# Performance work log

Hardware: AMD Instinct MI355X
Metric: run time of the kernel (lower is better)

Reference implementation:

```python
import jax, jax.numpy as jnp
import numpy as np

N = 200000
E = 600000
H = 128
OUT = 256
NUM_TYPES = 300
B = 128


def setup_inputs() -> dict:
    key = jax.random.key(0)
    ks = jax.random.split(key, 12)
    x = jax.random.randint(ks[0], (N,), 0, NUM_TYPES)
    edge_index = jax.random.randint(ks[1], (2, E), 0, N)
    batch = jnp.sort(jax.random.randint(ks[2], (N,), 0, B))
    s = 1.0 / np.sqrt(H)
    emb = jax.random.normal(ks[3], (NUM_TYPES, H), jnp.float32)
    W0 = jax.random.uniform(ks[4], (H, H), jnp.float32, -s, s)
    b0 = jax.random.uniform(ks[5], (H,), jnp.float32, -s, s)
    W1 = jax.random.uniform(ks[6], (H, H), jnp.float32, -s, s)
    b1 = jax.random.uniform(ks[7], (H,), jnp.float32, -s, s)
    Wo = jax.random.uniform(ks[8], (H, OUT), jnp.float32, -s, s)
    bo = jax.random.uniform(ks[9], (OUT,), jnp.float32, -s, s)
    gamma = jnp.ones((OUT,), jnp.float32)
    beta = jnp.zeros((OUT,), jnp.float32)
    return {"x": x, "edge_index": edge_index, "batch": batch, "batch_size": B,
            "emb": emb, "W0": W0, "b0": b0, "W1": W1, "b1": b1,
            "Wo": Wo, "bo": bo, "gamma": gamma, "beta": beta}


def gcn_layer(h, full_src, full_dst, W, b, n):
    # gather messages, scatter-add to destinations (bidirectional edges pre-built)
    msg = h[full_src]                                   # [2E, H]
    agg = jax.ops.segment_sum(msg, full_dst, num_segments=n)
    deg = jax.ops.segment_sum(jnp.ones((full_src.shape[0],), h.dtype),
                              full_dst, num_segments=n)
    deg = jnp.sqrt(jnp.clip(deg, 1.0))[:, None]
    out = agg / deg
    out = out @ W + b
    out = out + h
    return jax.nn.gelu(out, approximate=False)  # torch nn.GELU default is exact


def reference(x, edge_index, batch, batch_size, emb, W0, b0, W1, b1, Wo, bo, gamma, beta):
    n = x.shape[0]
    h = emb[x]                                          # [N, H] embedding gather
    src, dst = edge_index[0], edge_index[1]
    full_src = jnp.concatenate([src, dst])
    full_dst = jnp.concatenate([dst, src])
    h = gcn_layer(h, full_src, full_dst, W0, b0, n)
    h = gcn_layer(h, full_src, full_dst, W1, b1, n)
    # segment-mean pooling per graph
    gsum = jax.ops.segment_sum(h, batch, num_segments=batch_size)
    cnt = jax.ops.segment_sum(jnp.ones((n,), h.dtype), batch, num_segments=batch_size)
    gfeat = gsum / jnp.clip(cnt, 1.0)[:, None]
    out = gfeat @ Wo + bo
    mu = jnp.mean(out, axis=-1, keepdims=True)
    var = jnp.var(out, axis=-1, keepdims=True)
    out = (out - mu) * jax.lax.rsqrt(var + 1e-5) * gamma + beta
    return out
```

## Files before the change

### kernel.cpp

```cpp
#include <hip/hip_runtime.h>
#include <hip/hip_bf16.h>
#include <hip/hip_fp8.h>
#include <math.h>

#define H 128
#define OUTD 256
#define ASTRIDE 40
#define NODE_MASK 0x3FFFF

typedef unsigned short ushort_t;
typedef unsigned int uint_t;
typedef unsigned char uchar_t;
typedef __attribute__((ext_vector_type(8))) short short8;
typedef __attribute__((ext_vector_type(4))) float f32x4;
typedef __attribute__((ext_vector_type(2))) float f32x2;

__device__ __forceinline__ float bf2f(uint_t u){
    union { uint_t i; float f; } v; v.i = u << 16; return v.f;
}
__device__ __forceinline__ uint_t f2bf(float f){
    __hip_bfloat16 b = __float2bfloat16(f);
    union { __hip_bfloat16 b; ushort_t u; } v; v.b = b; return (uint_t)v.u;
}
__device__ __forceinline__ float fp8tof(uint_t u){
    __hip_fp8_e4m3 t; t.__x = (__hip_fp8_storage_t)u; return (float)t;
}
__device__ __forceinline__ uint_t ftofp8(float f){
    __hip_fp8_e4m3 t(f); return (uint_t)t.__x;
}
__device__ __forceinline__ uint_t pk2fp8(float a, float b){
#if __has_builtin(__builtin_amdgcn_cvt_pk_fp8_f32)
    return (uint_t)__builtin_amdgcn_cvt_pk_fp8_f32(a, b, 0, false) & 0xFFFFu;
#else
    return ftofp8(a) | (ftofp8(b) << 8);
#endif
}
__device__ __forceinline__ void acc_fp8(f32x4& v, uint_t u){
#if __has_builtin(__builtin_amdgcn_cvt_pk_f32_fp8)
    f32x2 lo = __builtin_amdgcn_cvt_pk_f32_fp8(u, false);
    f32x2 hi = __builtin_amdgcn_cvt_pk_f32_fp8(u, true);
    v[0] += lo[0]; v[1] += lo[1]; v[2] += hi[0]; v[3] += hi[1];
#else
    v[0] += fp8tof(u & 0xFFu);         v[1] += fp8tof((u >> 8) & 0xFFu);
    v[2] += fp8tof((u >> 16) & 0xFFu); v[3] += fp8tof(u >> 24);
#endif
}
__device__ __forceinline__ float gelu_fast(float x){
    float a = fabsf(x) * 0.70710678118654752440f;
    float t = __builtin_amdgcn_rcpf(fmaf(0.3275911f, a, 1.0f));
    float p = t*fmaf(t, fmaf(t, fmaf(t, fmaf(t, 1.061405429f, -1.453152027f),
                                     1.421413741f), -0.284496736f), 0.254829592f);
    float erf = 1.0f - p*__expf(-a*a);
    erf = copysignf(erf, x);
    return 0.5f * x * (1.0f + erf);
}

__global__ __launch_bounds__(256) void sniff_kernel(const ushort_t* __restrict__ data,
                                                    int count, int* __restrict__ flag_fp32){
    __shared__ float red[256];
    float m = 0.f;
    for (int i = threadIdx.x; i < count; i += 256){
        float v = fabsf(bf2f((uint_t)data[i]));
        if (isfinite(v)) m = fmaxf(m, v);
        else m = 1e30f;
    }
    red[threadIdx.x] = m;
    __syncthreads();
    #pragma unroll
    for (int s = 128; s > 0; s >>= 1){
        if (threadIdx.x < s) red[threadIdx.x] = fmaxf(red[threadIdx.x], red[threadIdx.x+s]);
        __syncthreads();
    }
    if (threadIdx.x == 0) *flag_fp32 = (red[0] > 100.f) ? 1 : 0;
}

struct StageArgs {
    const void* src[7];
    float*      dst[7];
    int         count[7];
    int         blk_off[8];
};
__global__ __launch_bounds__(256) void stage_all_kernel(StageArgs args,
                                                        const int* __restrict__ flag_fp32){
    int bx = blockIdx.x;
    int seg = 0;
    while (seg < 6 && bx >= args.blk_off[seg+1]) seg++;
    int idx = (bx - args.blk_off[seg])*256 + threadIdx.x;
    if (idx >= args.count[seg]) return;
    const int isf32 = *flag_fp32;
    args.dst[seg][idx] = isf32 ? ((const float*)args.src[seg])[idx]
                               : bf2f((uint_t)((const ushort_t*)args.src[seg])[idx]);
}

__global__ __launch_bounds__(256) void transpose_w_kernel(
        const void* __restrict__ Ws0, const void* __restrict__ Ws1,
        const void* __restrict__ embsrc, int szEmb,
        ushort_t* __restrict__ d0, ushort_t* __restrict__ d1,
        ushort_t* __restrict__ dEmb, uchar_t* __restrict__ dEmb8,
        int* __restrict__ zero_base, int zero_count,
        const int* __restrict__ flag_fp32){
    if (blockIdx.y == 3){
        for (int i = blockIdx.x*256 + threadIdx.x; i < zero_count; i += gridDim.x*256)
            zero_base[i] = 0;
        return;
    }
    const int isf32 = *flag_fp32;
    if (blockIdx.y == 2){
        int i = blockIdx.x*256 + threadIdx.x;
        if (i >= szEmb) return;
        ushort_t bv = isf32 ? (ushort_t)f2bf(((const float*)embsrc)[i])
                            : ((const ushort_t*)embsrc)[i];
        dEmb[i] = bv;
        int row = i >> 7, col = i & 127;
        int kb = col >> 5, qq = (col >> 3) & 3, jj = col & 7;
        dEmb8[(size_t)row*H + qq*32 + kb*8 + jj] = (uchar_t)ftofp8(bf2f((uint_t)bv));
        return;
    }
    const void* s = blockIdx.y ? Ws1 : Ws0;
    ushort_t*   d = blockIdx.y ? d1  : d0;
    int i = blockIdx.x*256 + threadIdx.x;
    if (i >= H*H) return;
    int k = i >> 7, nn = i & 127;
    ushort_t v = isf32 ? (ushort_t)f2bf(((const float*)s)[i])
                       : ((const ushort_t*)s)[i];
    d[nn*H + k] = v;
}

__global__ __launch_bounds__(256) void fill_part_kernel(const int* __restrict__ src,
        const int* __restrict__ dst, const int* __restrict__ x,
        int* __restrict__ deg, int* __restrict__ adj, int E, int n){
    int group = blockIdx.x & 7;
    int gblk  = blockIdx.x >> 3;
    int G     = gridDim.x >> 3;
    int lo = (int)(((long long)n * group) / 8);
    int hi = (int)(((long long)n * (group+1)) / 8);
    for (int e = gblk*256 + threadIdx.x; e < E; e += G*256){
        int s = src[e], d = dst[e];
        if (d >= lo && d < hi){
            int ts = x[s];
            int p = atomicAdd(&deg[d], 1);
            if (p < ASTRIDE) adj[(size_t)d*ASTRIDE + p] = s | (ts << 18);
        }
        if (s >= lo && s < hi){
            int td = x[d];
            int p = atomicAdd(&deg[s], 1);
            if (p < ASTRIDE) adj[(size_t)s*ASTRIDE + p] = d | (td << 18);
        }
    }
}

__global__ __launch_bounds__(512, 6) void gcn_fused(
    const int* __restrict__ deg, const int* __restrict__ adj,
    const ushort_t* __restrict__ gsrc, const uchar_t* __restrict__ g8,
    const int* __restrict__ xmap,
    const ushort_t* __restrict__ WT, const float* __restrict__ b,
    ushort_t* __restrict__ h_out, uchar_t* __restrict__ h8_out,
    int n, int use_x){
    __shared__ ushort_t Wt[128*136];
    for (int i = threadIdx.x; i < 2048; i += 512){
        int nn = i >> 4;
        int k0 = (i & 15) << 3;
        *(uint4*)(&Wt[nn*136 + k0]) = *(const uint4*)(WT + nn*H + k0);
    }
    __syncthreads();
    const int lane = threadIdx.x & 63;
    const int wave = threadIdx.x >> 6;
    const int quad = lane >> 4;
    const int lid  = lane & 15;

    int row = blockIdx.x*128 + wave*16 + lid;
    int cnt = (row < n) ? deg[row] : 0;
    float s = rsqrtf((float)(cnt < 1 ? 1 : cnt));
    if (cnt > ASTRIDE) cnt = ASTRIDE;
    const uint_t* ap = (const uint_t*)(adj + (size_t)row*ASTRIDE);

    f32x4 g[8];
    #pragma unroll
    for (int i=0;i<8;i++) g[i] = (f32x4){0.f,0.f,0.f,0.f};

    uint4 c0 = {0,0,0,0}, c1 = {0,0,0,0}, n0 = {0,0,0,0}, n1 = {0,0,0,0};
    if (cnt > 0){
        uint_t e = ap[0];
        size_t ro = (size_t)(use_x ? (e >> 18) : (e & NODE_MASK)) * H;
        const uchar_t* hp = g8 + ro + quad*32;
        c0 = *(const uint4*)(hp); c1 = *(const uint4*)(hp + 16);
    }
    if (cnt > 1){
        uint_t e = ap[1];
        size_t ro = (size_t)(use_x ? (e >> 18) : (e & NODE_MASK)) * H;
        const uchar_t* hp = g8 + ro + quad*32;
        n0 = *(const uint4*)(hp); n1 = *(const uint4*)(hp + 16);
    }
    for (int j=0; j<cnt; j++){
        uint4 f0 = {0,0,0,0}, f1 = {0,0,0,0};
        if (j+2 < cnt){
            uint_t e = ap[j+2];
            size_t ro = (size_t)(use_x ? (e >> 18) : (e & NODE_MASK)) * H;
            const uchar_t* hp = g8 + ro + quad*32;
            f0 = *(const uint4*)(hp); f1 = *(const uint4*)(hp + 16);
        }
        acc_fp8(g[0], c0.x); acc_fp8(g[1], c0.y);
        acc_fp8(g[2], c0.z); acc_fp8(g[3], c0.w);
        acc_fp8(g[4], c1.x); acc_fp8(g[5], c1.y);
        acc_fp8(g[6], c1.z); acc_fp8(g[7], c1.w);
        c0 = n0; c1 = n1; n0 = f0; n1 = f1;
    }

    short8 afrag[4];
    #pragma unroll
    for (int kb=0;kb<4;kb++){
        uint_t w0 = f2bf(g[2*kb][0]*s)   | (f2bf(g[2*kb][1]*s)   << 16);
        uint_t w1 = f2bf(g[2*kb][2]*s)   | (f2bf(g[2*kb][3]*s)   << 16);
        uint_t w2 = f2bf(g[2*kb+1][0]*s) | (f2bf(g[2*kb+1][1]*s) << 16);
        uint_t w3 = f2bf(g[2*kb+1][2]*s) | (f2bf(g[2*kb+1][3]*s) << 16);
        uint4 packed; packed.x=w0; packed.y=w1; packed.z=w2; packed.w=w3;
        afrag[kb] = *(short8*)&packed;
    }

    f32x4 acc[8];
    #pragma unroll
    for (int ct=0;ct<8;ct++) acc[ct] = (f32x4){0.f,0.f,0.f,0.f};
    #pragma unroll
    for (int kb=0;kb<4;kb++){
        #pragma unroll
        for (int ct=0;ct<8;ct++){
            short8 bf = *(const short8*)(&Wt[(ct*16+lid)*136 + kb*32 + quad*8]);
            acc[ct] = __builtin_amdgcn_mfma_f32_16x16x32_bf16(afrag[kb], bf, acc[ct], 0,0,0);
        }
    }

    float bcol[8];
    #pragma unroll
    for (int ct=0;ct<8;ct++) bcol[ct] = b[ct*16 + lid];
    int rowq = blockIdx.x*128 + wave*16 + quad*4;
    bool full = (blockIdx.x*128 + wave*16 + 16) <= n;
    const int boff = ((lid >> 3) << 5) + (lid & 7);
    #pragma unroll
    for (int r=0;r<4;r++){
        int grow = rowq + r;
        if (full || grow < n){
            if (use_x){
                const ushort_t* hr = gsrc + (size_t)xmap[grow]*H + lid;
                uchar_t* o8 = h8_out + (size_t)grow*H;
                float vv[8];
                #pragma unroll
                for (int ct=0;ct<8;ct++){
                    float hv = bf2f((uint_t)hr[ct*16]);
                    vv[ct] = gelu_fast(acc[ct][r] + bcol[ct] + hv);
                }
                #pragma unroll
                for (int cp=0;cp<4;cp++){
                    uint_t pk = pk2fp8(vv[2*cp], vv[2*cp+1]);
                    o8[boff + cp*8]      = (uchar_t)(pk & 0xFF);
                    o8[boff + 64 + cp*8] = (uchar_t)(pk >> 8);
                }
            } else {
                const uchar_t* h8r = g8 + (size_t)grow*H;
                ushort_t* orp = h_out + (size_t)grow*H + lid;
                #pragma unroll
                for (int ct=0;ct<8;ct++){
                    int off2 = boff + ((ct & 1) << 6) + ((ct >> 1) << 3);
                    float hv = fp8tof((uint_t)h8r[off2]);
                    float v  = gelu_fast(acc[ct][r] + bcol[ct] + hv);
                    orp[ct*16] = (ushort_t)f2bf(v);
                }
            }
        }
    }
}

__global__ __launch_bounds__(256) void pool_kernel(const ushort_t* __restrict__ h,
        const int* __restrict__ batch, float* __restrict__ gfeat, int n){
    int g = blockIdx.x;
    int q = blockIdx.y;
    __shared__ int se[2];
    if (threadIdx.x == 0){
        int lo=0, hi=n;
        while (lo<hi){ int m=(lo+hi)>>1; if (batch[m] < g) lo=m+1; else hi=m; }
        se[0] = lo;
        hi = n;
        while (lo<hi){ int m=(lo+hi)>>1; if (batch[m] <= g) lo=m+1; else hi=m; }
        se[1] = lo;
    }
    __syncthreads();
    int start = se[0], end = se[1];
    int chunk = (end - start + 3) >> 2;
    int s = start + q*chunk;
    int e = s + chunk; if (e > end) e = end;
    int col0 = (threadIdx.x & 15) << 3;
    int rg   = threadIdx.x >> 4;
    float acc[8];
    #pragma unroll
    for (int i=0;i<8;i++) acc[i] = 0.f;
    for (int r = s + rg; r < e; r += 16){
        uint4 raw = *(const uint4*)(h + (size_t)r*H + col0);
        acc[0] += bf2f(raw.x & 0xFFFFu); acc[1] += bf2f(raw.x >> 16);
        acc[2] += bf2f(raw.y & 0xFFFFu); acc[3] += bf2f(raw.y >> 16);
        acc[4] += bf2f(raw.z & 0xFFFFu); acc[5] += bf2f(raw.z >> 16);
        acc[6] += bf2f(raw.w & 0xFFFFu); acc[7] += bf2f(raw.w >> 16);
    }
    __shared__ float red[16][128];
    #pragma unroll
    for (int i=0;i<8;i++) red[rg][col0+i] = acc[i];
    __syncthreads();
    #pragma unroll
    for (int st=8; st>=1; st>>=1){
        if (rg < st){
            #pragma unroll
            for (int i=0;i<8;i++) red[rg][col0+i] += red[rg+st][col0+i];
        }
        __syncthreads();
    }
    if (rg == 0){
        #pragma unroll
        for (int i=0;i<8;i++) atomicAdd(&gfeat[(size_t)g*H + col0 + i], red[0][col0+i]);
    }
}

__global__ __launch_bounds__(256) void head_kernel(const float* __restrict__ gfeat,
        const int* __restrict__ batch, int n,
        const float* __restrict__ Wo, const float* __restrict__ bo,
        const float* __restrict__ gamma, const float* __restrict__ beta,
        void* __restrict__ out, const int* __restrict__ flag_fp32){
    int g = blockIdx.x;
    int j = threadIdx.x;
    __shared__ float gf[H];
    __shared__ float icnt_sh;
    if (j == 0){
        int lo=0, hi=n;
        while (lo<hi){ int m=(lo+hi)>>1; if (batch[m] < g) lo=m+1; else hi=m; }
        int st = lo;
        hi = n;
        while (lo<hi){ int m=(lo+hi)>>1; if (batch[m] <= g) lo=m+1; else hi=m; }
        int cnt = lo - st; if (cnt < 1) cnt = 1;
        icnt_sh = 1.0f / (float)cnt;
    }
    __syncthreads();
    if (j < H) gf[j] = gfeat[(size_t)g*H + j] * icnt_sh;
    __syncthreads();
    float acc = bo[j];
    #pragma unroll 8
    for (int k=0;k<H;k++) acc += gf[k] * Wo[(size_t)k*OUTD + j];
    __shared__ float red[256];
    red[j] = acc;
    __syncthreads();
    #pragma unroll
    for (int s2=128;s2>0;s2>>=1){
        if (j < s2) red[j] += red[j+s2];
        __syncthreads();
    }
    float mu = red[0] * (1.f/OUTD);
    __syncthreads();
    float d = acc - mu;
    red[j] = d*d;
    __syncthreads();
    #pragma unroll
    for (int s2=128;s2>0;s2>>=1){
        if (j < s2) red[j] += red[j+s2];
        __syncthreads();
    }
    float var = red[0] * (1.f/OUTD);
    float val = d * rsqrtf(var + 1e-5f) * gamma[j] + beta[j];
    size_t idx = (size_t)g*OUTD + j;
    if (*flag_fp32) ((float*)out)[idx] = val;
    else            ((ushort_t*)out)[idx] = (ushort_t)f2bf(val);
}

extern "C" void kernel_launch(void* const* d_in, const int* in_sizes, int n_in,
                              void* d_out, int out_size, void* d_ws, size_t ws_size,
                              hipStream_t stream){
    const int* x     = (const int*)d_in[0];
    const int* edge  = (const int*)d_in[1];
    const int* batch = (const int*)d_in[2];

    const int n = in_sizes[0];
    const int E = in_sizes[1] / 2;
    const int B = out_size / OUTD;
    const int* srcp = edge;
    const int* dstp = edge + E;

    const int szEmb = in_sizes[4], szb0 = in_sizes[6], szb1 = in_sizes[8];
    const int szWo = in_sizes[9], szbo = in_sizes[10], szg = in_sizes[11], szbt = in_sizes[12];

    char* base = (char*)d_ws;
    size_t off = 0;
    auto take = [&](size_t bytes)->char*{
        char* p = base + off;
        off = (off + bytes + 15) & ~(size_t)15;
        return p;
    };
    int*   flag   = (int*)  take(4);
    ushort_t* embb= (ushort_t*)take((size_t)szEmb*2);
    uchar_t* emb8 = (uchar_t*)take((size_t)szEmb);
    ushort_t* WT0 = (ushort_t*)take((size_t)H*H*2);
    ushort_t* WT1 = (ushort_t*)take((size_t)H*H*2);
    float* sb0    = (float*)take((size_t)szb0*4);
    float* sb1    = (float*)take((size_t)szb1*4);
    float* sWo    = (float*)take((size_t)szWo*4);
    float* sbo    = (float*)take((size_t)szbo*4);
    float* sg     = (float*)take((size_t)szg*4);
    float* sbt    = (float*)take((size_t)szbt*4);
    int*   adj    = (int*)  take((size_t)n*ASTRIDE*4);
    ushort_t* hA  = (ushort_t*)take((size_t)n*H*2);
    uchar_t*  h8  = (uchar_t*)take((size_t)n*H);
    char* zbase   = take((size_t)n*4 + (size_t)B*H*4);
    int*   deg    = (int*)zbase;
    float* gfeat  = (float*)(zbase + (size_t)n*4);
    const int zero_ints = n + B*H;

    sniff_kernel<<<1, 256, 0, stream>>>((const ushort_t*)d_in[4], szEmb, flag);

    StageArgs sa;
    const void* ssrc[7] = {d_in[9], d_in[6], d_in[8], d_in[10], d_in[11], d_in[12], d_in[10]};
    float*      sdst[7] = {sWo, sb0, sb1, sbo, sg, sbt, sbo};
    int         scnt[7] = {szWo, szb0, szb1, szbo, szg, szbt, 0};
    int run = 0;
    for (int i=0;i<7;i++){
        sa.src[i] = ssrc[i]; sa.dst[i] = sdst[i]; sa.count[i] = scnt[i];
        sa.blk_off[i] = run; run += (scnt[i] + 255)/256;
    }
    sa.blk_off[7] = run;
    stage_all_kernel<<<run, 256, 0, stream>>>(sa, flag);
    int tgrid = ((H*H > szEmb ? H*H : szEmb) + 255)/256;
    transpose_w_kernel<<<dim3(tgrid, 4), 256, 0, stream>>>(d_in[5], d_in[7],
                                                           d_in[4], szEmb,
                                                           WT0, WT1, embb, emb8,
                                                           (int*)zbase, zero_ints, flag);

    fill_part_kernel<<<2048, 256, 0, stream>>>(srcp, dstp, x, deg, adj, E, n);

    const int nblk = (n + 127) / 128;
    gcn_fused<<<nblk, 512, 0, stream>>>(deg, adj, embb, emb8, x,
                                        WT0, sb0, (ushort_t*)nullptr, h8, n, 1);
    gcn_fused<<<nblk, 512, 0, stream>>>(deg, adj, embb, h8, x,
                                        WT1, sb1, hA, (uchar_t*)nullptr, n, 0);

    pool_kernel<<<dim3(B,4), 256, 0, stream>>>(hA, batch, gfeat, n);
    head_kernel<<<B, 256, 0, stream>>>(gfeat, batch, n, sWo, sbo, sg, sbt, d_out, flag);
}
```

Baseline: 351.8 us.

## Fuse mean-pool into second GCN layer and batch-prefetch neighbor gathers

The second GCN layer now adds its GELU outputs straight into per-block shared-memory pooling bins, falling back to global atomics for graphs outside the bins. This removes the bf16 hidden-state write and the separate pool kernel. The neighbor gather loads adjacency entries in vector chunks and issues four row gathers ahead, unrolled for the first 12 edges. The kernel is also templated on USE_X and launch bounds change from 6 to 4 blocks per SM, which trades occupancy for registers and adds shared-memory atomic contention.

```diff
diff --git a/kernel.cpp b/kernel.cpp
--- a/kernel.cpp
+++ b/kernel.cpp
@@ -7,6 +7,7 @@
 #define OUTD 256
 #define ASTRIDE 40
 #define NODE_MASK 0x3FFFF
+#define PBINS 4
 
 typedef unsigned short ushort_t;
 typedef unsigned int uint_t;
@@ -39,7 +40,9 @@
 #if __has_builtin(__builtin_amdgcn_cvt_pk_f32_fp8)
     f32x2 lo = __builtin_amdgcn_cvt_pk_f32_fp8(u, false);
     f32x2 hi = __builtin_amdgcn_cvt_pk_f32_fp8(u, true);
-    v[0] += lo[0]; v[1] += lo[1]; v[2] += hi[0]; v[3] += hi[1];
+    f32x2 a = {v[0], v[1]}, b2 = {v[2], v[3]};
+    a += lo; b2 += hi;
+    v = (f32x4){a[0], a[1], b2[0], b2[1]};
 #else
     v[0] += fp8tof(u & 0xFFu);         v[1] += fp8tof((u >> 8) & 0xFFu);
     v[2] += fp8tof((u >> 16) & 0xFFu); v[3] += fp8tof(u >> 24);
@@ -149,18 +152,37 @@
     }
 }
 
-__global__ __launch_bounds__(512, 6) void gcn_fused(
+#define GLOAD(E, RA, RB) do { \
+    size_t ro_ = (size_t)(USE_X ? ((E) >> 18) : ((E) & NODE_MASK)) * H; \
+    const uchar_t* hp_ = g8 + ro_ + quad*32; \
+    RA = *(const uint4*)(hp_); RB = *(const uint4*)(hp_ + 16); } while(0)
+
+#define GACC(RA, RB) do { \
+    acc_fp8(g[0], RA.x); acc_fp8(g[1], RA.y); \
+    acc_fp8(g[2], RA.z); acc_fp8(g[3], RA.w); \
+    acc_fp8(g[4], RB.x); acc_fp8(g[5], RB.y); \
+    acc_fp8(g[6], RB.z); acc_fp8(g[7], RB.w); } while(0)
+
+template<int USE_X>
+__global__ __launch_bounds__(512, 4) void gcn_fused(
     const int* __restrict__ deg, const int* __restrict__ adj,
     const ushort_t* __restrict__ gsrc, const uchar_t* __restrict__ g8,
     const int* __restrict__ xmap,
     const ushort_t* __restrict__ WT, const float* __restrict__ b,
-    ushort_t* __restrict__ h_out, uchar_t* __restrict__ h8_out,
-    int n, int use_x){
+    uchar_t* __restrict__ h8_out,
+    const int* __restrict__ batchp, float* __restrict__ gfeat,
+    int n){
     __shared__ ushort_t Wt[128*136];
+    __shared__ float poolsh[PBINS*H];
+    __shared__ int bg0sh;
     for (int i = threadIdx.x; i < 2048; i += 512){
         int nn = i >> 4;
         int k0 = (i & 15) << 3;
         *(uint4*)(&Wt[nn*136 + k0]) = *(const uint4*)(WT + nn*H + k0);
+    }
+    if (!USE_X){
+        for (int i = threadIdx.x; i < PBINS*H; i += 512) poolsh[i] = 0.f;
+        if (threadIdx.x == 0) bg0sh = batchp[blockIdx.x*128];
     }
     __syncthreads();
     const int lane = threadIdx.x & 63;
@@ -178,32 +200,35 @@
     #pragma unroll
     for (int i=0;i<8;i++) g[i] = (f32x4){0.f,0.f,0.f,0.f};
 
-    uint4 c0 = {0,0,0,0}, c1 = {0,0,0,0}, n0 = {0,0,0,0}, n1 = {0,0,0,0};
-    if (cnt > 0){
-        uint_t e = ap[0];
-        size_t ro = (size_t)(use_x ? (e >> 18) : (e & NODE_MASK)) * H;
-        const uchar_t* hp = g8 + ro + quad*32;
-        c0 = *(const uint4*)(hp); c1 = *(const uint4*)(hp + 16);
-    }
-    if (cnt > 1){
-        uint_t e = ap[1];
-        size_t ro = (size_t)(use_x ? (e >> 18) : (e & NODE_MASK)) * H;
-        const uchar_t* hp = g8 + ro + quad*32;
-        n0 = *(const uint4*)(hp); n1 = *(const uint4*)(hp + 16);
-    }
-    for (int j=0; j<cnt; j++){
-        uint4 f0 = {0,0,0,0}, f1 = {0,0,0,0};
-        if (j+2 < cnt){
-            uint_t e = ap[j+2];
-            size_t ro = (size_t)(use_x ? (e >> 18) : (e & NODE_MASK)) * H;
-            const uchar_t* hp = g8 + ro + quad*32;
-            f0 = *(const uint4*)(hp); f1 = *(const uint4*)(hp + 16);
-        }
-        acc_fp8(g[0], c0.x); acc_fp8(g[1], c0.y);
-        acc_fp8(g[2], c0.z); acc_fp8(g[3], c0.w);
-        acc_fp8(g[4], c1.x); acc_fp8(g[5], c1.y);
-        acc_fp8(g[6], c1.z); acc_fp8(g[7], c1.w);
-        c0 = n0; c1 = n1; n0 = f0; n1 = f1;
+    uint4 ew0 = {0,0,0,0}, ew1 = {0,0,0,0}, ew2 = {0,0,0,0};
+    if (row < n){
+        ew0 = *(const uint4*)(ap);
+        ew1 = *(const uint4*)(ap + 4);
+        ew2 = *(const uint4*)(ap + 8);
+    }
+
+    uint4 pA0, pA1, pB0, pB1, pC0, pC1, pD0, pD1;
+    if (cnt > 0) GLOAD(ew0.x, pA0, pA1);
+    if (cnt > 1) GLOAD(ew0.y, pB0, pB1);
+    if (cnt > 2) GLOAD(ew0.z, pC0, pC1);
+    if (cnt > 3) GLOAD(ew0.w, pD0, pD1);
+    if (cnt > 0){ GACC(pA0, pA1); if (cnt > 4) GLOAD(ew1.x, pA0, pA1); }
+    if (cnt > 1){ GACC(pB0, pB1); if (cnt > 5) GLOAD(ew1.y, pB0, pB1); }
+    if (cnt > 2){ GACC(pC0, pC1); if (cnt > 6) GLOAD(ew1.z, pC0, pC1); }
+    if (cnt > 3){ GACC(pD0, pD1); if (cnt > 7) GLOAD(ew1.w, pD0, pD1); }
+    if (cnt > 4){ GACC(pA0, pA1); if (cnt > 8)  GLOAD(ew2.x, pA0, pA1); }
+    if (cnt > 5){ GACC(pB0, pB1); if (cnt > 9)  GLOAD(ew2.y, pB0, pB1); }
+    if (cnt > 6){ GACC(pC0, pC1); if (cnt > 10) GLOAD(ew2.z, pC0, pC1); }
+    if (cnt > 7){ GACC(pD0, pD1); if (cnt > 11) GLOAD(ew2.w, pD0, pD1); }
+    if (cnt > 8)  GACC(pA0, pA1);
+    if (cnt > 9)  GACC(pB0, pB1);
+    if (cnt > 10) GACC(pC0, pC1);
+    if (cnt > 11) GACC(pD0, pD1);
+    for (int j = 12; j < cnt; j++){
+        uint_t e = ap[j];
+        uint4 t0, t1;
+        GLOAD(e, t0, t1);
+        GACC(t0, t1);
     }
 
     short8 afrag[4];
@@ -239,7 +264,7 @@
     for (int r=0;r<4;r++){
         int grow = rowq + r;
         if (full || grow < n){
-            if (use_x){
+            if (USE_X){
                 const ushort_t* hr = gsrc + (size_t)xmap[grow]*H + lid;
                 uchar_t* o8 = h8_out + (size_t)grow*H;
                 float vv[8];
@@ -256,64 +281,28 @@
                 }
             } else {
                 const uchar_t* h8r = g8 + (size_t)grow*H;
-                ushort_t* orp = h_out + (size_t)grow*H + lid;
+                int gbid = batchp[grow];
+                int gi = gbid - bg0sh;
+                bool inl = (gi >= 0) && (gi < PBINS);
                 #pragma unroll
                 for (int ct=0;ct<8;ct++){
                     int off2 = boff + ((ct & 1) << 6) + ((ct >> 1) << 3);
                     float hv = fp8tof((uint_t)h8r[off2]);
                     float v  = gelu_fast(acc[ct][r] + bcol[ct] + hv);
-                    orp[ct*16] = (ushort_t)f2bf(v);
+                    int col = ct*16 + lid;
+                    if (inl) atomicAdd(&poolsh[gi*H + col], v);
+                    else     atomicAdd(&gfeat[(size_t)gbid*H + col], v);
                 }
             }
         }
     }
-}
-
-__global__ __launch_bounds__(256) void pool_kernel(const ushort_t* __restrict__ h,
-        const int* __restrict__ batch, float* __restrict__ gfeat, int n){
-    int g = blockIdx.x;
-    int q = blockIdx.y;
-    __shared__ int se[2];
-    if (threadIdx.x == 0){
-        int lo=0, hi=n;
-        while (lo<hi){ int m=(lo+hi)>>1; if (batch[m] < g) lo=m+1; else hi=m; }
-        se[0] = lo;
-        hi = n;
-        while (lo<hi){ int m=(lo+hi)>>1; if (batch[m] <= g) lo=m+1; else hi=m; }
-        se[1] = lo;
-    }
-    __syncthreads();
-    int start = se[0], end = se[1];
-    int chunk = (end - start + 3) >> 2;
-    int s = start + q*chunk;
-    int e = s + chunk; if (e > end) e = end;
-    int col0 = (threadIdx.x & 15) << 3;
-    int rg   = threadIdx.x >> 4;
-    float acc[8];
-    #pragma unroll
-    for (int i=0;i<8;i++) acc[i] = 0.f;
-    for (int r = s + rg; r < e; r += 16){
-        uint4 raw = *(const uint4*)(h + (size_t)r*H + col0);
-        acc[0] += bf2f(raw.x & 0xFFFFu); acc[1] += bf2f(raw.x >> 16);
-        acc[2] += bf2f(raw.y & 0xFFFFu); acc[3] += bf2f(raw.y >> 16);
-        acc[4] += bf2f(raw.z & 0xFFFFu); acc[5] += bf2f(raw.z >> 16);
-        acc[6] += bf2f(raw.w & 0xFFFFu); acc[7] += bf2f(raw.w >> 16);
-    }
-    __shared__ float red[16][128];
-    #pragma unroll
-    for (int i=0;i<8;i++) red[rg][col0+i] = acc[i];
-    __syncthreads();
-    #pragma unroll
-    for (int st=8; st>=1; st>>=1){
-        if (rg < st){
-            #pragma unroll
-            for (int i=0;i<8;i++) red[rg][col0+i] += red[rg+st][col0+i];
-        }
+
+    if (!USE_X){
         __syncthreads();
-    }
-    if (rg == 0){
-        #pragma unroll
-        for (int i=0;i<8;i++) atomicAdd(&gfeat[(size_t)g*H + col0 + i], red[0][col0+i]);
+        int i = threadIdx.x;
+        float v = poolsh[i];
+        if (v != 0.f)
+            atomicAdd(&gfeat[(size_t)(bg0sh + (i >> 7))*H + (i & 127)], v);
     }
 }
 
@@ -401,7 +390,6 @@
     float* sg     = (float*)take((size_t)szg*4);
     float* sbt    = (float*)take((size_t)szbt*4);
     int*   adj    = (int*)  take((size_t)n*ASTRIDE*4);
-    ushort_t* hA  = (ushort_t*)take((size_t)n*H*2);
     uchar_t*  h8  = (uchar_t*)take((size_t)n*H);
     char* zbase   = take((size_t)n*4 + (size_t)B*H*4);
     int*   deg    = (int*)zbase;
@@ -430,11 +418,12 @@
     fill_part_kernel<<<2048, 256, 0, stream>>>(srcp, dstp, x, deg, adj, E, n);
 
     const int nblk = (n + 127) / 128;
-    gcn_fused<<<nblk, 512, 0, stream>>>(deg, adj, embb, emb8, x,
-                                        WT0, sb0, (ushort_t*)nullptr, h8, n, 1);
-    gcn_fused<<<nblk, 512, 0, stream>>>(deg, adj, embb, h8, x,
-                                        WT1, sb1, hA, (uchar_t*)nullptr, n, 0);
-
-    pool_kernel<<<dim3(B,4), 256, 0, stream>>>(hA, batch, gfeat, n);
+    gcn_fused<1><<<nblk, 512, 0, stream>>>(deg, adj, embb, emb8, x,
+                                           WT0, sb0, h8,
+                                           (const int*)nullptr, (float*)nullptr, n);
+    gcn_fused<0><<<nblk, 512, 0, stream>>>(deg, adj, embb, h8, x,
+                                           WT1, sb1, (uchar_t*)nullptr,
+                                           batch, gfeat, n);
+
     head_kernel<<<B, 256, 0, stream>>>(gfeat, batch, n, sWo, sbo, sg, sbt, d_out, flag);
 }
```

Result: slower. 420.4 us (+19.5%).
